# Optimization experiments

Measured on AMD Instinct MI355X. Metric: run time of the kernel, lower is better.

## Reference

```python
import jax, jax.numpy as jnp
import numpy as np

B = 4096
N = 4097  # num_samples; basis fit uses N-1 columns


def _trapz_cumsum(x, t):
    # y[..., 0] = 0; y[..., i] = y[..., i-1] + 0.5*(t[i]-t[i-1])*(x[..., i-1]+x[..., i])
    dt = t[1:] - t[:-1]                                   # (N-1,)
    inc = 0.5 * dt * (x[..., :-1] + x[..., 1:])           # (B,1,N-1)
    zero = jnp.zeros(x.shape[:-1] + (1,), x.dtype)
    return jnp.concatenate([zero, jnp.cumsum(inc, axis=-1)], axis=-1)  # (B,1,N)


def setup_inputs() -> dict:
    key = jax.random.key(0)
    k1, k2 = jax.random.split(key)
    # positive signal so ny + cumsum(x) stays > 0 (needed for pow/log)
    x = jax.random.uniform(k1, (B, 1, N), dtype=jnp.float32, minval=0.1, maxval=1.1)
    # strictly increasing time grid
    dt = jax.random.uniform(k2, (N,), dtype=jnp.float32, minval=1e-3, maxval=1e-2)
    t = jnp.cumsum(dt)
    params = jnp.array([0.5, 1.0], dtype=jnp.float32)  # [r, ny]
    return {"x": x, "t": t, "params": params}


def reference(x, t, params):
    r, ny = params[0], params[1]
    y = _trapz_cumsum(x, t)                  # (B,1,N)
    z = ny + y[:, 0, 1:]                     # (B,N-1)
    phi = jnp.stack([z, z ** r], axis=1)     # (B,2,N-1)  basis matrix
    phip = jnp.linalg.pinv(phi)              # (B,N-1,2)
    x_sl = x[:, :, 1:]                       # (B,1,N-1)
    coeffs = x_sl @ phip                     # (B,1,2)
    x_hat = coeffs @ phi                     # (B,1,N-1)
    res = x_sl - x_hat                       # (B,1,N-1)
    r2 = jnp.sum(res ** 2, axis=-1)          # (B,1)
    return coeffs, x_hat, res, r2
```

## Files before the change

kernel.cpp:

```cpp
#include <hip/hip_runtime.h>

typedef float f32x4 __attribute__((ext_vector_type(4)));

constexpr int NPTS = 4097;
constexpr int M    = 4096;
constexpr int TPB  = 256;
constexpr int NW   = TPB / 64;
constexpr int NJ   = 4;

template<int S>
__device__ __forceinline__ void load_scan(
    const float* __restrict__ xrow, const float* __restrict__ t,
    int tid, int lane,
    float (&xs)[NJ][4], float (&zl)[NJ][4], float (&gs)[NJ])
{
    const float* __restrict__ xal = xrow - S;
#pragma unroll
    for (int j = 0; j < NJ; ++j) {
        const int e = j * 1024 + tid * 4;
        const f32x4 a4 = *reinterpret_cast<const f32x4*>(xal + e);
        const f32x4 c4 = *reinterpret_cast<const f32x4*>(xal + e + 4);
        const float cmb[8] = {a4.x, a4.y, a4.z, a4.w, c4.x, c4.y, c4.z, c4.w};
        const float x0 = cmb[S + 0], x1 = cmb[S + 1], x2 = cmb[S + 2],
                    x3 = cmb[S + 3], x4 = cmb[S + 4];

        const f32x4 tq = *reinterpret_cast<const f32x4*>(t + e);
        float tn = __shfl_down(tq.x, 1, 64);
        if (lane == 63) tn = t[e + 4];

        const float i0 = 0.5f * (tq.y - tq.x) * (x0 + x1);
        const float i1 = 0.5f * (tq.z - tq.y) * (x1 + x2);
        const float i2 = 0.5f * (tq.w - tq.z) * (x2 + x3);
        const float i3 = 0.5f * (tn   - tq.w) * (x3 + x4);
        zl[j][0] = i0;
        zl[j][1] = i0 + i1;
        zl[j][2] = i0 + i1 + i2;
        zl[j][3] = i0 + i1 + i2 + i3;
        gs[j] = zl[j][3];
        xs[j][0] = x1; xs[j][1] = x2; xs[j][2] = x3; xs[j][3] = x4;
    }
}

__global__ __launch_bounds__(TPB)
void vp_kernel(const float* __restrict__ x, const float* __restrict__ t,
               const float* __restrict__ params, float* __restrict__ out, int B)
{
    const int b    = blockIdx.x;
    const int tid  = threadIdx.x;
    const int lane = tid & 63;
    const int wid  = tid >> 6;

    const float r  = params[0];
    const float ny = params[1];

    const float* __restrict__ xrow = x + (size_t)b * NPTS;

    __shared__ float  wt[NW][NJ];
    __shared__ double wred[NW][6];

    float xs[NJ][4];
    float zl[NJ][4];
    float gs[NJ];

    switch (b & 3) {
    case 0: load_scan<0>(xrow, t, tid, lane, xs, zl, gs); break;
    case 1: load_scan<1>(xrow, t, tid, lane, xs, zl, gs); break;
    case 2: load_scan<2>(xrow, t, tid, lane, xs, zl, gs); break;
    default: load_scan<3>(xrow, t, tid, lane, xs, zl, gs); break;
    }

    float sc0 = gs[0], sc1 = gs[1], sc2 = gs[2], sc3 = gs[3];
#pragma unroll
    for (int d = 1; d < 64; d <<= 1) {
        float u0 = __shfl_up(sc0, d, 64);
        float u1 = __shfl_up(sc1, d, 64);
        float u2 = __shfl_up(sc2, d, 64);
        float u3 = __shfl_up(sc3, d, 64);
        if (lane >= d) { sc0 += u0; sc1 += u1; sc2 += u2; sc3 += u3; }
    }

    if (lane == 63) {
        wt[wid][0] = sc0; wt[wid][1] = sc1; wt[wid][2] = sc2; wt[wid][3] = sc3;
    }
    __syncthreads();

    float woff[NJ] = {0, 0, 0, 0};
    float Tj[NJ]   = {0, 0, 0, 0};
#pragma unroll
    for (int w = 0; w < NW; ++w) {
#pragma unroll
        for (int j = 0; j < NJ; ++j) {
            float v = wt[w][j];
            Tj[j] += v;
            if (w < wid) woff[j] += v;
        }
    }
    float zbase[NJ];
    float jacc = 0.f;
    const float scv[NJ] = {sc0, sc1, sc2, sc3};
#pragma unroll
    for (int j = 0; j < NJ; ++j) {
        zbase[j] = ny + jacc + woff[j] + (scv[j] - gs[j]);
        jacc += Tj[j];
    }

    double szz = 0, szw = 0, sww = 0, sxz = 0, sxw = 0;
#pragma unroll
    for (int j = 0; j < NJ; ++j) {
#pragma unroll
        for (int i = 0; i < 4; ++i) {
            float z = zbase[j] + zl[j][i];
            zl[j][i] = z;
            float w = (r == 0.5f) ? sqrtf(z) : powf(z, r);
            float xv = xs[j][i];
            szz += (double)z  * (double)z;
            szw += (double)z  * (double)w;
            sww += (double)w  * (double)w;
            sxz += (double)xv * (double)z;
            sxw += (double)xv * (double)w;
        }
    }
#pragma unroll
    for (int d = 32; d > 0; d >>= 1) {
        szz += __shfl_down(szz, d, 64);
        szw += __shfl_down(szw, d, 64);
        sww += __shfl_down(sww, d, 64);
        sxz += __shfl_down(sxz, d, 64);
        sxw += __shfl_down(sxw, d, 64);
    }
    if (lane == 0) {
        wred[wid][0] = szz; wred[wid][1] = szw; wred[wid][2] = sww;
        wred[wid][3] = sxz; wred[wid][4] = sxw;
    }
    __syncthreads();

    double a0 = 0, a1 = 0, a2 = 0, a3 = 0, a4 = 0;
#pragma unroll
    for (int w = 0; w < NW; ++w) {
        a0 += wred[w][0]; a1 += wred[w][1]; a2 += wred[w][2];
        a3 += wred[w][3]; a4 += wred[w][4];
    }
    {
        double det = a0 * a2 - a1 * a1;
        double inv = 1.0 / det;
        double c0d = (a3 * a2 - a4 * a1) * inv;
        double c1d = (a4 * a0 - a3 * a1) * inv;
        if (tid == 0) {
            out[(size_t)b * 2 + 0] = (float)c0d;
            out[(size_t)b * 2 + 1] = (float)c1d;
        }
        const float c0 = (float)c0d, c1 = (float)c1d;

        float* __restrict__ xhat = out + (size_t)B * 2 + (size_t)b * M;
        float* __restrict__ res  = xhat + (size_t)B * M;

        double r2 = 0;
#pragma unroll
        for (int j = 0; j < NJ; ++j) {
            const int e = j * 1024 + tid * 4;
            float h[4], ev[4];
#pragma unroll
            for (int i = 0; i < 4; ++i) {
                float z = zl[j][i];
                float w = (r == 0.5f) ? sqrtf(z) : powf(z, r);
                h[i]  = c0 * z + c1 * w;
                ev[i] = xs[j][i] - h[i];
                r2 += (double)ev[i] * (double)ev[i];
            }
            f32x4 hv = {h[0], h[1], h[2], h[3]};
            f32x4 rv = {ev[0], ev[1], ev[2], ev[3]};
            __builtin_nontemporal_store(hv, reinterpret_cast<f32x4*>(xhat + e));
            __builtin_nontemporal_store(rv, reinterpret_cast<f32x4*>(res + e));
        }
#pragma unroll
        for (int d = 32; d > 0; d >>= 1) r2 += __shfl_down(r2, d, 64);
        if (lane == 0) wred[wid][5] = r2;
        __syncthreads();
        if (tid == 0) {
            double s = 0;
            for (int w = 0; w < NW; ++w) s += wred[w][5];
            out[(size_t)B * 2 + 2 * (size_t)B * M + b] = (float)s;
        }
    }
}

extern "C" void kernel_launch(void* const* d_in, const int* in_sizes, int n_in,
                              void* d_out, int out_size, void* d_ws, size_t ws_size,
                              hipStream_t stream) {
    const float* x = (const float*)d_in[0];
    const float* t = (const float*)d_in[1];
    const float* p = (const float*)d_in[2];
    float* out     = (float*)d_out;
    const int B    = in_sizes[0] / NPTS;

    vp_kernel<<<dim3(B), dim3(TPB), 0, stream>>>(x, t, p, out, B);
}
```

Baseline: 49.88 us.

## Process two rows per block and move Gram reductions to fp32

Each block now handles two consecutive rows, so the time-grid loads and dt computation are shared and there are twice as many independent scans and reductions per thread for latency hiding. Per-thread Gram and residual accumulation switches from double to float with fmaf, with partials summed in double only at the end. The r==0.5 branch is hoisted into a template parameter, and the nontemporal stores become plain stores. This cuts FP64 work and block count, but raises register pressure, may lower occupancy, and reduces accumulation precision.

```diff
diff --git a/kernel.cpp b/kernel.cpp
--- a/kernel.cpp
+++ b/kernel.cpp
@@ -7,37 +7,214 @@
 constexpr int TPB  = 256;
 constexpr int NW   = TPB / 64;
 constexpr int NJ   = 4;
+constexpr int ROWS = 2;
+constexpr int NC   = ROWS * NJ;
+
+struct Lds {
+    float wt[NW][NC];
+    float gram[NW][ROWS * 5];
+    float r2s[NW][ROWS];
+};
 
 template<int S>
-__device__ __forceinline__ void load_scan(
-    const float* __restrict__ xrow, const float* __restrict__ t,
-    int tid, int lane,
-    float (&xs)[NJ][4], float (&zl)[NJ][4], float (&gs)[NJ])
+__device__ __forceinline__ void scan4(const f32x4 a, const f32x4 c,
+                                      float d0, float d1, float d2, float d3,
+                                      float (&xsj)[4], float (&zlj)[4], float& gsj)
 {
-    const float* __restrict__ xal = xrow - S;
+    const float m[8] = {a.x, a.y, a.z, a.w, c.x, c.y, c.z, c.w};
+    const float x0 = m[S+0], x1 = m[S+1], x2 = m[S+2], x3 = m[S+3], x4 = m[S+4];
+    const float i0 = d0 * (x0 + x1);
+    const float i1 = d1 * (x1 + x2);
+    const float i2 = d2 * (x2 + x3);
+    const float i3 = d3 * (x3 + x4);
+    zlj[0] = i0;
+    zlj[1] = i0 + i1;
+    zlj[2] = zlj[1] + i2;
+    zlj[3] = zlj[2] + i3;
+    gsj = zlj[3];
+    xsj[0] = x1; xsj[1] = x2; xsj[2] = x3; xsj[3] = x4;
+}
+
+template<int S0, bool RHALF>
+__device__ __forceinline__ void body(const float* __restrict__ x,
+                                     const float* __restrict__ t,
+                                     float r, float ny,
+                                     float* __restrict__ out,
+                                     int b0, int B, Lds& L)
+{
+    constexpr int S1 = S0 + 1;
+    const int tid  = threadIdx.x;
+    const int lane = tid & 63;
+    const int wid  = tid >> 6;
+
+    const float* __restrict__ xal0 = x + (size_t)b0 * NPTS - S0;
+    const float* __restrict__ xal1 = x + (size_t)(b0 + 1) * NPTS - S1;
+
+    float xs[ROWS][NJ][4];
+    float zl[ROWS][NJ][4];
+    float gs[NC];
+
 #pragma unroll
     for (int j = 0; j < NJ; ++j) {
         const int e = j * 1024 + tid * 4;
-        const f32x4 a4 = *reinterpret_cast<const f32x4*>(xal + e);
-        const f32x4 c4 = *reinterpret_cast<const f32x4*>(xal + e + 4);
-        const float cmb[8] = {a4.x, a4.y, a4.z, a4.w, c4.x, c4.y, c4.z, c4.w};
-        const float x0 = cmb[S + 0], x1 = cmb[S + 1], x2 = cmb[S + 2],
-                    x3 = cmb[S + 3], x4 = cmb[S + 4];
-
-        const f32x4 tq = *reinterpret_cast<const f32x4*>(t + e);
+        const f32x4 xa0 = *(const f32x4*)(xal0 + e);
+        const f32x4 xc0 = *(const f32x4*)(xal0 + e + 4);
+        const f32x4 xa1 = *(const f32x4*)(xal1 + e);
+        const f32x4 xc1 = *(const f32x4*)(xal1 + e + 4);
+        const f32x4 tq  = *(const f32x4*)(t + e);
         float tn = __shfl_down(tq.x, 1, 64);
         if (lane == 63) tn = t[e + 4];
-
-        const float i0 = 0.5f * (tq.y - tq.x) * (x0 + x1);
-        const float i1 = 0.5f * (tq.z - tq.y) * (x1 + x2);
-        const float i2 = 0.5f * (tq.w - tq.z) * (x2 + x3);
-        const float i3 = 0.5f * (tn   - tq.w) * (x3 + x4);
-        zl[j][0] = i0;
-        zl[j][1] = i0 + i1;
-        zl[j][2] = i0 + i1 + i2;
-        zl[j][3] = i0 + i1 + i2 + i3;
-        gs[j] = zl[j][3];
-        xs[j][0] = x1; xs[j][1] = x2; xs[j][2] = x3; xs[j][3] = x4;
+        const float d0 = 0.5f * (tq.y - tq.x);
+        const float d1 = 0.5f * (tq.z - tq.y);
+        const float d2 = 0.5f * (tq.w - tq.z);
+        const float d3 = 0.5f * (tn   - tq.w);
+        scan4<S0>(xa0, xc0, d0, d1, d2, d3, xs[0][j], zl[0][j], gs[0 * NJ + j]);
+        scan4<S1>(xa1, xc1, d0, d1, d2, d3, xs[1][j], zl[1][j], gs[1 * NJ + j]);
+    }
+
+    float sc[NC];
+#pragma unroll
+    for (int c = 0; c < NC; ++c) sc[c] = gs[c];
+#pragma unroll
+    for (int d = 1; d < 64; d <<= 1) {
+#pragma unroll
+        for (int c = 0; c < NC; ++c) {
+            float u = __shfl_up(sc[c], d, 64);
+            if (lane >= d) sc[c] += u;
+        }
+    }
+    if (lane == 63) {
+#pragma unroll
+        for (int c = 0; c < NC; ++c) L.wt[wid][c] = sc[c];
+    }
+    __syncthreads();
+
+    float woff[NC] = {}, Tt[NC] = {};
+#pragma unroll
+    for (int w = 0; w < NW; ++w) {
+#pragma unroll
+        for (int c = 0; c < NC; ++c) {
+            const float v = L.wt[w][c];
+            Tt[c] += v;
+            if (w < wid) woff[c] += v;
+        }
+    }
+
+    float zb[ROWS][NJ];
+#pragma unroll
+    for (int R = 0; R < ROWS; ++R) {
+        float jacc = 0.f;
+#pragma unroll
+        for (int j = 0; j < NJ; ++j) {
+            const int c = R * NJ + j;
+            zb[R][j] = ny + jacc + woff[c] + (sc[c] - gs[c]);
+            jacc += Tt[c];
+        }
+    }
+
+    float s[ROWS][5];
+#pragma unroll
+    for (int R = 0; R < ROWS; ++R)
+#pragma unroll
+        for (int k = 0; k < 5; ++k) s[R][k] = 0.f;
+
+#pragma unroll
+    for (int R = 0; R < ROWS; ++R) {
+#pragma unroll
+        for (int j = 0; j < NJ; ++j) {
+            float pzz = 0, pzw = 0, pww = 0, pxz = 0, pxw = 0;
+#pragma unroll
+            for (int i = 0; i < 4; ++i) {
+                const float z = zb[R][j] + zl[R][j][i];
+                zl[R][j][i] = z;
+                const float w = RHALF ? sqrtf(z) : powf(z, r);
+                const float xv = xs[R][j][i];
+                pzz = fmaf(z,  z, pzz);
+                pzw = fmaf(z,  w, pzw);
+                pww = fmaf(w,  w, pww);
+                pxz = fmaf(xv, z, pxz);
+                pxw = fmaf(xv, w, pxw);
+            }
+            s[R][0] += pzz; s[R][1] += pzw; s[R][2] += pww;
+            s[R][3] += pxz; s[R][4] += pxw;
+        }
+    }
+#pragma unroll
+    for (int d = 32; d > 0; d >>= 1)
+#pragma unroll
+        for (int R = 0; R < ROWS; ++R)
+#pragma unroll
+            for (int k = 0; k < 5; ++k)
+                s[R][k] += __shfl_down(s[R][k], d, 64);
+
+    if (lane == 0) {
+#pragma unroll
+        for (int R = 0; R < ROWS; ++R)
+#pragma unroll
+            for (int k = 0; k < 5; ++k) L.gram[wid][R * 5 + k] = s[R][k];
+    }
+    __syncthreads();
+
+    float c0[ROWS], c1[ROWS];
+#pragma unroll
+    for (int R = 0; R < ROWS; ++R) {
+        double a0 = 0, a1 = 0, a2 = 0, a3 = 0, a4 = 0;
+#pragma unroll
+        for (int w = 0; w < NW; ++w) {
+            a0 += L.gram[w][R * 5 + 0];
+            a1 += L.gram[w][R * 5 + 1];
+            a2 += L.gram[w][R * 5 + 2];
+            a3 += L.gram[w][R * 5 + 3];
+            a4 += L.gram[w][R * 5 + 4];
+        }
+        const double det = a0 * a2 - a1 * a1;
+        const double inv = 1.0 / det;
+        const double cc0 = (a3 * a2 - a4 * a1) * inv;
+        const double cc1 = (a4 * a0 - a3 * a1) * inv;
+        c0[R] = (float)cc0;
+        c1[R] = (float)cc1;
+        if (tid == R) {
+            out[(size_t)(b0 + R) * 2 + 0] = (float)cc0;
+            out[(size_t)(b0 + R) * 2 + 1] = (float)cc1;
+        }
+    }
+
+    float r2[ROWS] = {};
+#pragma unroll
+    for (int R = 0; R < ROWS; ++R) {
+        float* __restrict__ xhat = out + (size_t)B * 2 + (size_t)(b0 + R) * M;
+        float* __restrict__ res  = xhat + (size_t)B * M;
+#pragma unroll
+        for (int j = 0; j < NJ; ++j) {
+            const int e = j * 1024 + tid * 4;
+            f32x4 hv, rv;
+#pragma unroll
+            for (int i = 0; i < 4; ++i) {
+                const float z = zl[R][j][i];
+                const float w = RHALF ? sqrtf(z) : powf(z, r);
+                const float h  = c0[R] * z + c1[R] * w;
+                const float ev = xs[R][j][i] - h;
+                hv[i] = h; rv[i] = ev;
+                r2[R] = fmaf(ev, ev, r2[R]);
+            }
+            *(f32x4*)(xhat + e) = hv;
+            *(f32x4*)(res  + e) = rv;
+        }
+    }
+#pragma unroll
+    for (int d = 32; d > 0; d >>= 1)
+#pragma unroll
+        for (int R = 0; R < ROWS; ++R) r2[R] += __shfl_down(r2[R], d, 64);
+    if (lane == 0) {
+        L.r2s[wid][0] = r2[0];
+        L.r2s[wid][1] = r2[1];
+    }
+    __syncthreads();
+    if (tid < ROWS) {
+        float acc = 0.f;
+#pragma unroll
+        for (int w = 0; w < NW; ++w) acc += L.r2s[w][tid];
+        out[(size_t)B * 2 + 2 * (size_t)B * M + (b0 + tid)] = acc;
     }
 }
 
@@ -45,142 +222,18 @@
 void vp_kernel(const float* __restrict__ x, const float* __restrict__ t,
                const float* __restrict__ params, float* __restrict__ out, int B)
 {
-    const int b    = blockIdx.x;
-    const int tid  = threadIdx.x;
-    const int lane = tid & 63;
-    const int wid  = tid >> 6;
-
+    __shared__ Lds L;
     const float r  = params[0];
     const float ny = params[1];
-
-    const float* __restrict__ xrow = x + (size_t)b * NPTS;
-
-    __shared__ float  wt[NW][NJ];
-    __shared__ double wred[NW][6];
-
-    float xs[NJ][4];
-    float zl[NJ][4];
-    float gs[NJ];
-
-    switch (b & 3) {
-    case 0: load_scan<0>(xrow, t, tid, lane, xs, zl, gs); break;
-    case 1: load_scan<1>(xrow, t, tid, lane, xs, zl, gs); break;
-    case 2: load_scan<2>(xrow, t, tid, lane, xs, zl, gs); break;
-    default: load_scan<3>(xrow, t, tid, lane, xs, zl, gs); break;
-    }
-
-    float sc0 = gs[0], sc1 = gs[1], sc2 = gs[2], sc3 = gs[3];
-#pragma unroll
-    for (int d = 1; d < 64; d <<= 1) {
-        float u0 = __shfl_up(sc0, d, 64);
-        float u1 = __shfl_up(sc1, d, 64);
-        float u2 = __shfl_up(sc2, d, 64);
-        float u3 = __shfl_up(sc3, d, 64);
-        if (lane >= d) { sc0 += u0; sc1 += u1; sc2 += u2; sc3 += u3; }
-    }
-
-    if (lane == 63) {
-        wt[wid][0] = sc0; wt[wid][1] = sc1; wt[wid][2] = sc2; wt[wid][3] = sc3;
-    }
-    __syncthreads();
-
-    float woff[NJ] = {0, 0, 0, 0};
-    float Tj[NJ]   = {0, 0, 0, 0};
-#pragma unroll
-    for (int w = 0; w < NW; ++w) {
-#pragma unroll
-        for (int j = 0; j < NJ; ++j) {
-            float v = wt[w][j];
-            Tj[j] += v;
-            if (w < wid) woff[j] += v;
-        }
-    }
-    float zbase[NJ];
-    float jacc = 0.f;
-    const float scv[NJ] = {sc0, sc1, sc2, sc3};
-#pragma unroll
-    for (int j = 0; j < NJ; ++j) {
-        zbase[j] = ny + jacc + woff[j] + (scv[j] - gs[j]);
-        jacc += Tj[j];
-    }
-
-    double szz = 0, szw = 0, sww = 0, sxz = 0, sxw = 0;
-#pragma unroll
-    for (int j = 0; j < NJ; ++j) {
-#pragma unroll
-        for (int i = 0; i < 4; ++i) {
-            float z = zbase[j] + zl[j][i];
-            zl[j][i] = z;
-            float w = (r == 0.5f) ? sqrtf(z) : powf(z, r);
-            float xv = xs[j][i];
-            szz += (double)z  * (double)z;
-            szw += (double)z  * (double)w;
-            sww += (double)w  * (double)w;
-            sxz += (double)xv * (double)z;
-            sxw += (double)xv * (double)w;
-        }
-    }
-#pragma unroll
-    for (int d = 32; d > 0; d >>= 1) {
-        szz += __shfl_down(szz, d, 64);
-        szw += __shfl_down(szw, d, 64);
-        sww += __shfl_down(sww, d, 64);
-        sxz += __shfl_down(sxz, d, 64);
-        sxw += __shfl_down(sxw, d, 64);
-    }
-    if (lane == 0) {
-        wred[wid][0] = szz; wred[wid][1] = szw; wred[wid][2] = sww;
-        wred[wid][3] = sxz; wred[wid][4] = sxw;
-    }
-    __syncthreads();
-
-    double a0 = 0, a1 = 0, a2 = 0, a3 = 0, a4 = 0;
-#pragma unroll
-    for (int w = 0; w < NW; ++w) {
-        a0 += wred[w][0]; a1 += wred[w][1]; a2 += wred[w][2];
-        a3 += wred[w][3]; a4 += wred[w][4];
-    }
-    {
-        double det = a0 * a2 - a1 * a1;
-        double inv = 1.0 / det;
-        double c0d = (a3 * a2 - a4 * a1) * inv;
-        double c1d = (a4 * a0 - a3 * a1) * inv;
-        if (tid == 0) {
-            out[(size_t)b * 2 + 0] = (float)c0d;
-            out[(size_t)b * 2 + 1] = (float)c1d;
-        }
-        const float c0 = (float)c0d, c1 = (float)c1d;
-
-        float* __restrict__ xhat = out + (size_t)B * 2 + (size_t)b * M;
-        float* __restrict__ res  = xhat + (size_t)B * M;
-
-        double r2 = 0;
-#pragma unroll
-        for (int j = 0; j < NJ; ++j) {
-            const int e = j * 1024 + tid * 4;
-            float h[4], ev[4];
-#pragma unroll
-            for (int i = 0; i < 4; ++i) {
-                float z = zl[j][i];
-                float w = (r == 0.5f) ? sqrtf(z) : powf(z, r);
-                h[i]  = c0 * z + c1 * w;
-                ev[i] = xs[j][i] - h[i];
-                r2 += (double)ev[i] * (double)ev[i];
-            }
-            f32x4 hv = {h[0], h[1], h[2], h[3]};
-            f32x4 rv = {ev[0], ev[1], ev[2], ev[3]};
-            __builtin_nontemporal_store(hv, reinterpret_cast<f32x4*>(xhat + e));
-            __builtin_nontemporal_store(rv, reinterpret_cast<f32x4*>(res + e));
-        }
-#pragma unroll
-        for (int d = 32; d > 0; d >>= 1) r2 += __shfl_down(r2, d, 64);
-        if (lane == 0) wred[wid][5] = r2;
-        __syncthreads();
-        if (tid == 0) {
-            double s = 0;
-            for (int w = 0; w < NW; ++w) s += wred[w][5];
-            out[(size_t)B * 2 + 2 * (size_t)B * M + b] = (float)s;
-        }
+    const int  b0  = blockIdx.x * 2;
+    const bool odd = blockIdx.x & 1;
+
+    if (r == 0.5f) {
+        if (odd) body<2, true >(x, t, r, ny, out, b0, B, L);
+        else     body<0, true >(x, t, r, ny, out, b0, B, L);
+    } else {
+        if (odd) body<2, false>(x, t, r, ny, out, b0, B, L);
+        else     body<0, false>(x, t, r, ny, out, b0, B, L);
     }
 }
 
@@ -193,5 +246,5 @@
     float* out     = (float*)d_out;
     const int B    = in_sizes[0] / NPTS;
 
-    vp_kernel<<<dim3(B), dim3(TPB), 0, stream>>>(x, t, p, out, B);
-}
+    vp_kernel<<<dim3(B / 2), dim3(TPB), 0, stream>>>(x, t, p, out, B);
+}
```

Result: faster. 48.51 us, median of 3 (-2.7%).
